# Kernel optimization log

Measured on AMD Instinct MI355X. Metric: run time of the kernel, lower is better.

The kernel has to match this reference:

```python
import jax, jax.numpy as jnp
import numpy as np

FEATURE_DIM = 128  # user_aae.feature_dim == item_aae.feature_dim


def _encode(row, W1, b1, W2, b2):
    # row = [feature | x_rest]; original concatenates x and feature before the encoder MLP
    feat = row[:, :FEATURE_DIM]
    xr = row[:, FEATURE_DIM:]
    h = jax.nn.relu(jnp.concatenate([xr, feat], axis=-1) @ W1 + b1)
    return h @ W2 + b2  # [B, latent]


def setup_inputs() -> dict:
    key = jax.random.key(0)
    ks = jax.random.split(key, 12)
    B, NU, NI = 8192, 50000, 50000
    ROW, H, L = 2128, 512, 256  # feature_dim(128) + x_dim(2000)
    x = jnp.stack([
        jax.random.randint(ks[0], (B,), 0, NU),
        jax.random.randint(ks[1], (B,), 0, NI),
    ], axis=1).astype(jnp.int64)
    s1 = 1.0 / np.sqrt(ROW)
    s2 = 1.0 / np.sqrt(H)
    return {
        "x": x,
        "user_lookup": jax.random.normal(ks[2], (NU, ROW), jnp.float32),
        "item_lookup": jax.random.normal(ks[3], (NI, ROW), jnp.float32),
        "uW1": jax.random.normal(ks[4], (ROW, H), jnp.float32) * s1,
        "ub1": jnp.zeros((H,), jnp.float32),
        "uW2": jax.random.normal(ks[5], (H, L), jnp.float32) * s2,
        "ub2": jnp.zeros((L,), jnp.float32),
        "iW1": jax.random.normal(ks[6], (ROW, H), jnp.float32) * s1,
        "ib1": jnp.zeros((H,), jnp.float32),
        "iW2": jax.random.normal(ks[7], (H, L), jnp.float32) * s2,
        "ib2": jnp.zeros((L,), jnp.float32),
    }


def reference(x, user_lookup, item_lookup, uW1, ub1, uW2, ub2, iW1, ib1, iW2, ib2):
    user_row = user_lookup[x[:, 0]]  # [B, ROW]
    item_row = item_lookup[x[:, 1]]  # [B, ROW]
    u = _encode(user_row, uW1, ub1, uW2, ub2)  # [B, L]
    v = _encode(item_row, iW1, ib1, iW2, ib2)  # [B, L]
    # diag(u @ v.T) == rowwise dot product (identical math, no B x B matrix)
    diag = jnp.sum(u * v, axis=-1)
    return diag[:, None]  # [B, 1]
```

## Files before the change

### kernel.cpp

```cpp
#include <hip/hip_runtime.h>
#include <stdint.h>

typedef __attribute__((ext_vector_type(8))) short bf16x8;
typedef __attribute__((ext_vector_type(4))) float f32x4;

#define MFMA16(a, b, c) __builtin_amdgcn_mfma_f32_16x16x32_bf16((a), (b), (c), 0, 0, 0)

static __device__ __forceinline__ unsigned f2bf(float f) {
  union { float f; unsigned u; } cv;
  cv.f = f;
  return (cv.u + 0x7fffu + ((cv.u >> 16) & 1u)) >> 16;
}

#define BATCH 8192
#define ROWD  2128
#define HID   512
#define LATD  256
#define KC1   272
#define NT1   68
#define HSL_TW (BATCH * HID)

__device__ __forceinline__ void tcast_body(
    const float* __restrict__ in, unsigned short* __restrict__ o,
    int s, int N, int lgN, int Kin, int perm)
{
  const int kc = s >> lgN, n = s & (N - 1);
  unsigned short v[8];
#pragma unroll
  for (int e = 0; e < 8; ++e) {
    const int k = kc * 8 + e;
    float f = 0.0f;
    if (k < Kin) {
      const int src = perm ? (k < 128 ? k + 2000 : k - 128) : k;
      f = in[(size_t)src * N + n];
    }
    v[e] = (unsigned short)f2bf(f);
  }
  *(uint4*)(o + (size_t)s * 8) = *(const uint4*)v;
}

__global__ __launch_bounds__(256) void ASAECF_tcast(
    const float* __restrict__ uW1, const float* __restrict__ iW1,
    const float* __restrict__ uW2, const float* __restrict__ iW2,
    unsigned short* __restrict__ w1s, unsigned short* __restrict__ w2s)
{
  const int tower = blockIdx.z;
  const int s = blockIdx.x * 256 + threadIdx.x;
  if (blockIdx.y == 0) {
    tcast_body(tower ? iW1 : uW1, w1s + (size_t)tower * KC1 * HID * 8,
               s, HID, 9, ROWD, 1);
  } else {
    if (blockIdx.x >= 64) return;
    tcast_body(tower ? iW2 : uW2, w2s + (size_t)tower * 64 * LATD * 8,
               s, LATD, 8, HID, 0);
  }
}

__global__ __launch_bounds__(512) void ASAECF_gemm1(
    const int* __restrict__ x,
    const float* __restrict__ ulook, const float* __restrict__ ilook,
    const unsigned short* __restrict__ w1s,
    const float* __restrict__ ub1, const float* __restrict__ ib1,
    unsigned short* __restrict__ hsl)
{
  const int bid   = blockIdx.x;
  const int xcd   = bid & 7;
  const int idx   = bid >> 3;
  const int tower = xcd >> 2;
  const int nh    = idx & 1;
  const int mb    = (xcd & 3) * 16 + (idx >> 1);

  const float* __restrict__ look = tower ? ilook : ulook;
  const unsigned short* __restrict__ w1 = w1s + (size_t)tower * KC1 * HID * 8;
  const float* __restrict__ b1 = tower ? ib1 : ub1;
  unsigned short* __restrict__ hout = hsl + (size_t)tower * HSL_TW;

  __shared__ unsigned short Ab[2][128 * 40];

  const int tid  = threadIdx.x;
  const int lane = tid & 63, wid = tid >> 6;
  const int fr   = lane & 15, fq = lane >> 4;
  const int row0 = mb * 128;

  const int ar = tid >> 2, ak = (tid & 3) * 8;
  const long long arow = (long long)x[(row0 + ar) * 2 + tower] * ROWD + ak;

  int boff[2];
#pragma unroll
  for (int n = 0; n < 2; ++n)
    boff[n] = (fq * 512 + nh * 256 + wid * 32 + n * 16 + fr) * 8;

  struct A8 { f32x4 a, b; };
  auto loadA = [&](int tt) -> A8 {
    A8 v;
    v.a = f32x4{0.0f, 0.0f, 0.0f, 0.0f};
    v.b = f32x4{0.0f, 0.0f, 0.0f, 0.0f};
    if (tt * 32 + ak + 8 <= ROWD) {
      v.a = *(const f32x4*)(look + arow + tt * 32);
      v.b = *(const f32x4*)(look + arow + tt * 32 + 4);
    }
    return v;
  };
  auto writeA = [&](int buf, A8 v) {
    uint2 p, q;
    p.x = f2bf(v.a[0]) | (f2bf(v.a[1]) << 16);
    p.y = f2bf(v.a[2]) | (f2bf(v.a[3]) << 16);
    q.x = f2bf(v.b[0]) | (f2bf(v.b[1]) << 16);
    q.y = f2bf(v.b[2]) | (f2bf(v.b[3]) << 16);
    *(uint2*)&Ab[buf][ar * 40 + ak] = p;
    *(uint2*)&Ab[buf][ar * 40 + ak + 4] = q;
  };

  f32x4 acc[8][2] = {};
  bf16x8 bgc[2], bgn[2];
  A8 rA0, rA1;

  writeA(0, loadA(0));
  rA0 = loadA(1);
  rA1 = loadA(2);
#pragma unroll
  for (int n = 0; n < 2; ++n) bgc[n] = *(const bf16x8*)(w1 + boff[n]);

#pragma unroll 2
  for (int t = 0; t < NT1; ++t) {
    __syncthreads();
    const int cu = t & 1;

    const unsigned short* bpn = w1 + (size_t)(t + 1) * (4 * 512 * 8);
#pragma unroll
    for (int n = 0; n < 2; ++n) bgn[n] = *(const bf16x8*)(bpn + boff[n]);

    bf16x8 af[8];
#pragma unroll
    for (int m = 0; m < 8; ++m)
      af[m] = *(const bf16x8*)&Ab[cu][(m * 16 + fr) * 40 + fq * 8];
#pragma unroll
    for (int n = 0; n < 2; ++n)
#pragma unroll
      for (int m = 0; m < 8; ++m)
        acc[m][n] = MFMA16(af[m], bgc[n], acc[m][n]);

    if (cu == 0) { writeA(1, rA0); rA0 = loadA(t + 3); }
    else         { writeA(0, rA1); rA1 = loadA(t + 3); }

#pragma unroll
    for (int n = 0; n < 2; ++n) bgc[n] = bgn[n];
  }

#pragma unroll
  for (int n = 0; n < 2; ++n) {
    const int col = nh * 256 + wid * 32 + n * 16 + fr;
    const int kc = col >> 3, e = col & 7;
    const float bb = b1[col];
#pragma unroll
    for (int m = 0; m < 8; ++m)
#pragma unroll
      for (int i = 0; i < 4; ++i) {
        const int rowib = m * 16 + fq * 4 + i;
        const int chunk = mb * 2 + (rowib >> 6);
        const int row = rowib & 63;
        const float v = fmaxf(acc[m][n][i] + bb, 0.0f);
        hout[(((size_t)chunk * 64 + kc) * 64 + row) * 8 + e] = (unsigned short)f2bf(v);
      }
  }
}

__global__ __launch_bounds__(512, 2) void ASAECF_gemm2dot(
    const unsigned short* __restrict__ hsl,
    const unsigned short* __restrict__ w2s,
    const float* __restrict__ ub2, const float* __restrict__ ib2,
    float* __restrict__ out)
{
  const int tid  = threadIdx.x;
  const int lane = tid & 63, wid = tid >> 6;
  const int fr   = lane & 15, fq = lane >> 4;
  const int rb   = blockIdx.x;
  const int row0 = rb * 32;

  const unsigned short* __restrict__ hu = hsl;
  const unsigned short* __restrict__ hv = hsl + (size_t)HSL_TW;
  const size_t abase = ((size_t)(rb >> 1) * 64) * 64 * 8;
  const int lrow0 = (rb & 1) * 32;

  f32x4 au[2][2] = {}, av[2][2] = {};

#pragma unroll
  for (int t = 0; t < 8; ++t) {
#pragma unroll
    for (int s = 0; s < 2; ++s) {
      const int kc = t * 8 + s * 4 + fq;
      bf16x8 a_u[2], a_v[2], b_u[2], b_v[2];
#pragma unroll
      for (int m = 0; m < 2; ++m) {
        const size_t off = abase + ((size_t)kc * 64 + lrow0 + m * 16 + fr) * 8;
        a_u[m] = *(const bf16x8*)(hu + off);
        a_v[m] = *(const bf16x8*)(hv + off);
      }
#pragma unroll
      for (int n = 0; n < 2; ++n) {
        const int col = wid * 32 + n * 16 + fr;
        const size_t offb = ((size_t)kc * 256 + col) * 8;
        b_u[n] = *(const bf16x8*)(w2s + offb);
        b_v[n] = *(const bf16x8*)(w2s + (size_t)64 * 256 * 8 + offb);
      }
#pragma unroll
      for (int m = 0; m < 2; ++m)
#pragma unroll
        for (int n = 0; n < 2; ++n) {
          au[m][n] = MFMA16(a_u[m], b_u[n], au[m][n]);
          av[m][n] = MFMA16(a_v[m], b_v[n], av[m][n]);
        }
    }
  }

  __shared__ float red[8][32];
  float bu[2], bv[2];
#pragma unroll
  for (int n = 0; n < 2; ++n) {
    const int col = wid * 32 + n * 16 + fr;
    bu[n] = ub2[col];
    bv[n] = ib2[col];
  }
#pragma unroll
  for (int m = 0; m < 2; ++m)
#pragma unroll
    for (int i = 0; i < 4; ++i) {
      float p = 0.0f;
#pragma unroll
      for (int n = 0; n < 2; ++n)
        p += (au[m][n][i] + bu[n]) * (av[m][n][i] + bv[n]);
      p += __shfl_xor(p, 1, 64);
      p += __shfl_xor(p, 2, 64);
      p += __shfl_xor(p, 4, 64);
      p += __shfl_xor(p, 8, 64);
      if (fr == 0) red[wid][m * 16 + fq * 4 + i] = p;
    }
  __syncthreads();
  if (tid < 32) {
    float s = 0.0f;
#pragma unroll
    for (int w = 0; w < 8; ++w) s += red[w][tid];
    out[row0 + tid] = s;
  }
}

extern "C" void kernel_launch(void* const* d_in, const int* in_sizes, int n_in,
                              void* d_out, int out_size, void* d_ws, size_t ws_size,
                              hipStream_t stream) {
  (void)in_sizes; (void)n_in; (void)out_size; (void)ws_size;
  const int*   x     = (const int*)d_in[0];
  const float* ulook = (const float*)d_in[1];
  const float* ilook = (const float*)d_in[2];
  const float* uW1   = (const float*)d_in[3];
  const float* ub1   = (const float*)d_in[4];
  const float* uW2   = (const float*)d_in[5];
  const float* ub2   = (const float*)d_in[6];
  const float* iW1   = (const float*)d_in[7];
  const float* ib1   = (const float*)d_in[8];
  const float* iW2   = (const float*)d_in[9];
  const float* ib2   = (const float*)d_in[10];
  float* out = (float*)d_out;

  char* ws = (char*)d_ws;
  unsigned short* w1s = (unsigned short*)(ws);
  unsigned short* w2s = (unsigned short*)(ws + 4456448);
  unsigned short* hsl = (unsigned short*)(ws + 4980736);

  ASAECF_tcast<<<dim3(544, 2, 2), 256, 0, stream>>>(uW1, iW1, uW2, iW2, w1s, w2s);
  ASAECF_gemm1<<<dim3(256), 512, 0, stream>>>(x, ulook, ilook, w1s, ub1, ib1, hsl);
  ASAECF_gemm2dot<<<dim3(256), 512, 0, stream>>>(hsl, w2s, ub2, ib2, out);
}
```

Before: 77.75 us.

## Pre-gather and bf16-cast lookup rows, stage A via direct global-to-LDS loads

Adds a separate kernel that gathers the embedding rows for each batch index and casts them to bf16 into a padded dense workspace buffer. gemm1 then streams A tiles straight into LDS with global_load_lds instead of loading fp32 into registers, converting, and storing. This is meant to halve the A traffic inside the GEMM and remove conversion and register pressure from its main loop. The cost is an extra launch and a round trip of the gathered bf16 matrix through HBM. The unpadded LDS stride may also cause bank conflicts on the fragment reads.

After: 115.9 us. 49.1% more time.

```diff
diff --git a/kernel.cpp b/kernel.cpp
--- a/kernel.cpp
+++ b/kernel.cpp
@@ -5,6 +5,12 @@
 typedef __attribute__((ext_vector_type(4))) float f32x4;
 
 #define MFMA16(a, b, c) __builtin_amdgcn_mfma_f32_16x16x32_bf16((a), (b), (c), 0, 0, 0)
+
+__device__ __forceinline__ void gload_lds16(const void* g, void* l) {
+  __builtin_amdgcn_global_load_lds((const __attribute__((address_space(1))) void*)g,
+                                   (__attribute__((address_space(3))) void*)l,
+                                   16, 0, 0);
+}
 
 static __device__ __forceinline__ unsigned f2bf(float f) {
   union { float f; unsigned u; } cv;
@@ -14,6 +20,7 @@
 
 #define BATCH 8192
 #define ROWD  2128
+#define KP1   2176
 #define HID   512
 #define LATD  256
 #define KC1   272
@@ -56,9 +63,34 @@
   }
 }
 
-__global__ __launch_bounds__(512) void ASAECF_gemm1(
+__global__ __launch_bounds__(256) void ASAECF_agather(
     const int* __restrict__ x,
     const float* __restrict__ ulook, const float* __restrict__ ilook,
+    unsigned short* __restrict__ Ad)
+{
+  const int tower = blockIdx.y;
+  const int row   = blockIdx.x * 4 + (threadIdx.x >> 6);
+  const int lane  = threadIdx.x & 63;
+  const float* __restrict__ look = tower ? ilook : ulook;
+  const long long src = (long long)x[row * 2 + tower] * ROWD;
+  unsigned short* dst = Ad + ((size_t)tower * BATCH + row) * KP1;
+
+#pragma unroll
+  for (int c = 0; c < 9; ++c) {
+    const int k = c * 256 + lane * 4;
+    if (c == 8 && lane >= 32) break;
+    f32x4 v = {0.0f, 0.0f, 0.0f, 0.0f};
+    if (k + 4 <= ROWD)
+      v = __builtin_nontemporal_load((const f32x4*)(look + src + k));
+    uint2 p;
+    p.x = f2bf(v[0]) | (f2bf(v[1]) << 16);
+    p.y = f2bf(v[2]) | (f2bf(v[3]) << 16);
+    *(uint2*)(dst + k) = p;
+  }
+}
+
+__global__ __launch_bounds__(512) void ASAECF_gemm1(
+    const unsigned short* __restrict__ Ad,
     const unsigned short* __restrict__ w1s,
     const float* __restrict__ ub1, const float* __restrict__ ib1,
     unsigned short* __restrict__ hsl)
@@ -70,61 +102,41 @@
   const int nh    = idx & 1;
   const int mb    = (xcd & 3) * 16 + (idx >> 1);
 
-  const float* __restrict__ look = tower ? ilook : ulook;
+  const unsigned short* __restrict__ Adt = Ad + (size_t)tower * BATCH * KP1;
   const unsigned short* __restrict__ w1 = w1s + (size_t)tower * KC1 * HID * 8;
   const float* __restrict__ b1 = tower ? ib1 : ub1;
   unsigned short* __restrict__ hout = hsl + (size_t)tower * HSL_TW;
 
-  __shared__ unsigned short Ab[2][128 * 40];
+  __shared__ unsigned short Ab[2][128 * 32];
 
   const int tid  = threadIdx.x;
   const int lane = tid & 63, wid = tid >> 6;
   const int fr   = lane & 15, fq = lane >> 4;
   const int row0 = mb * 128;
 
-  const int ar = tid >> 2, ak = (tid & 3) * 8;
-  const long long arow = (long long)x[(row0 + ar) * 2 + tower] * ROWD + ak;
+  const unsigned short* asrc =
+      Adt + (size_t)(row0 + wid * 16 + (lane >> 2)) * KP1 + (lane & 3) * 8;
+  auto stageA = [&](int t, int buf) {
+    gload_lds16(asrc + t * 32, (char*)&Ab[buf][0] + wid * 1024 + lane * 16);
+  };
 
   int boff[2];
 #pragma unroll
   for (int n = 0; n < 2; ++n)
     boff[n] = (fq * 512 + nh * 256 + wid * 32 + n * 16 + fr) * 8;
 
-  struct A8 { f32x4 a, b; };
-  auto loadA = [&](int tt) -> A8 {
-    A8 v;
-    v.a = f32x4{0.0f, 0.0f, 0.0f, 0.0f};
-    v.b = f32x4{0.0f, 0.0f, 0.0f, 0.0f};
-    if (tt * 32 + ak + 8 <= ROWD) {
-      v.a = *(const f32x4*)(look + arow + tt * 32);
-      v.b = *(const f32x4*)(look + arow + tt * 32 + 4);
-    }
-    return v;
-  };
-  auto writeA = [&](int buf, A8 v) {
-    uint2 p, q;
-    p.x = f2bf(v.a[0]) | (f2bf(v.a[1]) << 16);
-    p.y = f2bf(v.a[2]) | (f2bf(v.a[3]) << 16);
-    q.x = f2bf(v.b[0]) | (f2bf(v.b[1]) << 16);
-    q.y = f2bf(v.b[2]) | (f2bf(v.b[3]) << 16);
-    *(uint2*)&Ab[buf][ar * 40 + ak] = p;
-    *(uint2*)&Ab[buf][ar * 40 + ak + 4] = q;
-  };
-
   f32x4 acc[8][2] = {};
   bf16x8 bgc[2], bgn[2];
-  A8 rA0, rA1;
-
-  writeA(0, loadA(0));
-  rA0 = loadA(1);
-  rA1 = loadA(2);
+
+  stageA(0, 0);
 #pragma unroll
   for (int n = 0; n < 2; ++n) bgc[n] = *(const bf16x8*)(w1 + boff[n]);
+  __syncthreads();
 
 #pragma unroll 2
   for (int t = 0; t < NT1; ++t) {
-    __syncthreads();
     const int cu = t & 1;
+    if (t + 1 < NT1) stageA(t + 1, cu ^ 1);
 
     const unsigned short* bpn = w1 + (size_t)(t + 1) * (4 * 512 * 8);
 #pragma unroll
@@ -133,18 +145,17 @@
     bf16x8 af[8];
 #pragma unroll
     for (int m = 0; m < 8; ++m)
-      af[m] = *(const bf16x8*)&Ab[cu][(m * 16 + fr) * 40 + fq * 8];
+      af[m] = *(const bf16x8*)&Ab[cu][(m * 16 + fr) * 32 + fq * 8];
 #pragma unroll
     for (int n = 0; n < 2; ++n)
 #pragma unroll
       for (int m = 0; m < 8; ++m)
         acc[m][n] = MFMA16(af[m], bgc[n], acc[m][n]);
 
-    if (cu == 0) { writeA(1, rA0); rA0 = loadA(t + 3); }
-    else         { writeA(0, rA1); rA1 = loadA(t + 3); }
-
 #pragma unroll
     for (int n = 0; n < 2; ++n) bgc[n] = bgn[n];
+
+    __syncthreads();
   }
 
 #pragma unroll
@@ -265,8 +276,10 @@
   unsigned short* w1s = (unsigned short*)(ws);
   unsigned short* w2s = (unsigned short*)(ws + 4456448);
   unsigned short* hsl = (unsigned short*)(ws + 4980736);
+  unsigned short* Ad  = (unsigned short*)(ws + 21757952);
 
   ASAECF_tcast<<<dim3(544, 2, 2), 256, 0, stream>>>(uW1, iW1, uW2, iW2, w1s, w2s);
-  ASAECF_gemm1<<<dim3(256), 512, 0, stream>>>(x, ulook, ilook, w1s, ub1, ib1, hsl);
+  ASAECF_agather<<<dim3(2048, 2), 256, 0, stream>>>(x, ulook, ilook, Ad);
+  ASAECF_gemm1<<<dim3(256), 512, 0, stream>>>(Ad, w1s, ub1, ib1, hsl);
   ASAECF_gemm2dot<<<dim3(256), 512, 0, stream>>>(hsl, w2s, ub2, ib2, out);
 }
```

## Widen gemm1 K-step to 128 with larger LDS double buffers

Applied to the files above, without the earlier changes.

The gather-GEMM main loop now advances 128 K elements per iteration instead of 32, giving 17 iterations instead of 68. Each thread loads 32 contiguous floats per gathered row and prefetches four B slabs into registers. This cuts the number of block-wide barriers and issues longer contiguous gather loads, so more memory is in flight per round trip. In exchange it needs 80KB of dynamic LDS and many more registers per thread, which may lower occupancy or cause spills.

New measurement: 110.6 us. +42.3%, slower.

```diff
diff --git a/kernel.cpp b/kernel.cpp
--- a/kernel.cpp
+++ b/kernel.cpp
@@ -17,7 +17,10 @@
 #define HID   512
 #define LATD  256
 #define KC1   272
-#define NT1   68
+#define NTB   17
+#define SLAB  16384
+#define SUBT  5120
+#define ABUF  20480
 #define HSL_TW (BATCH * HID)
 
 __device__ __forceinline__ void tcast_body(
@@ -63,6 +66,8 @@
     const float* __restrict__ ub1, const float* __restrict__ ib1,
     unsigned short* __restrict__ hsl)
 {
+  extern __shared__ unsigned short Asl[];
+
   const int bid   = blockIdx.x;
   const int xcd   = bid & 7;
   const int idx   = bid >> 3;
@@ -75,76 +80,89 @@
   const float* __restrict__ b1 = tower ? ib1 : ub1;
   unsigned short* __restrict__ hout = hsl + (size_t)tower * HSL_TW;
 
-  __shared__ unsigned short Ab[2][128 * 40];
-
   const int tid  = threadIdx.x;
   const int lane = tid & 63, wid = tid >> 6;
   const int fr   = lane & 15, fq = lane >> 4;
   const int row0 = mb * 128;
 
-  const int ar = tid >> 2, ak = (tid & 3) * 8;
-  const long long arow = (long long)x[(row0 + ar) * 2 + tower] * ROWD + ak;
+  const int ar = tid >> 2, ks0 = tid & 3;
+  const long long arow = (long long)x[(row0 + ar) * 2 + tower] * ROWD + ks0 * 32;
+  unsigned short* awr = &Asl[0] ;
 
   int boff[2];
 #pragma unroll
   for (int n = 0; n < 2; ++n)
     boff[n] = (fq * 512 + nh * 256 + wid * 32 + n * 16 + fr) * 8;
 
-  struct A8 { f32x4 a, b; };
-  auto loadA = [&](int tt) -> A8 {
-    A8 v;
-    v.a = f32x4{0.0f, 0.0f, 0.0f, 0.0f};
-    v.b = f32x4{0.0f, 0.0f, 0.0f, 0.0f};
-    if (tt * 32 + ak + 8 <= ROWD) {
-      v.a = *(const f32x4*)(look + arow + tt * 32);
-      v.b = *(const f32x4*)(look + arow + tt * 32 + 4);
-    }
-    return v;
+  f32x4 rA[8];
+  auto loadA = [&](int t) {
+    const int kb = t * 128 + ks0 * 32;
+#pragma unroll
+    for (int j = 0; j < 8; ++j) {
+      rA[j] = f32x4{0.0f, 0.0f, 0.0f, 0.0f};
+      if (kb + j * 4 + 4 <= ROWD)
+        rA[j] = *(const f32x4*)(look + arow + t * 128 + j * 4);
+    }
   };
-  auto writeA = [&](int buf, A8 v) {
-    uint2 p, q;
-    p.x = f2bf(v.a[0]) | (f2bf(v.a[1]) << 16);
-    p.y = f2bf(v.a[2]) | (f2bf(v.a[3]) << 16);
-    q.x = f2bf(v.b[0]) | (f2bf(v.b[1]) << 16);
-    q.y = f2bf(v.b[2]) | (f2bf(v.b[3]) << 16);
-    *(uint2*)&Ab[buf][ar * 40 + ak] = p;
-    *(uint2*)&Ab[buf][ar * 40 + ak + 4] = q;
+  auto writeA = [&](int buf) {
+    unsigned short v[32];
+#pragma unroll
+    for (int j = 0; j < 8; ++j)
+#pragma unroll
+      for (int e = 0; e < 4; ++e)
+        v[j * 4 + e] = (unsigned short)f2bf(rA[j][e]);
+    unsigned short* d = &Asl[buf * ABUF + ks0 * SUBT + ar * 40];
+#pragma unroll
+    for (int c = 0; c < 4; ++c)
+      *(bf16x8*)(d + c * 8) = *(const bf16x8*)(v + c * 8);
   };
 
   f32x4 acc[8][2] = {};
-  bf16x8 bgc[2], bgn[2];
-  A8 rA0, rA1;
-
-  writeA(0, loadA(0));
-  rA0 = loadA(1);
-  rA1 = loadA(2);
-#pragma unroll
-  for (int n = 0; n < 2; ++n) bgc[n] = *(const bf16x8*)(w1 + boff[n]);
-
-#pragma unroll 2
-  for (int t = 0; t < NT1; ++t) {
+  bf16x8 Bc[4][2], Bn[4][2];
+
+  loadA(0);
+  writeA(0);
+#pragma unroll
+  for (int s = 0; s < 4; ++s)
+#pragma unroll
+    for (int n = 0; n < 2; ++n)
+      Bc[s][n] = *(const bf16x8*)(w1 + (size_t)s * SLAB + boff[n]);
+  __syncthreads();
+
+  for (int t = 0; t < NTB; ++t) {
+    const int cu = t & 1;
+    const bool pre = (t + 1 < NTB);
+    if (pre) {
+#pragma unroll
+      for (int s = 0; s < 4; ++s)
+#pragma unroll
+        for (int n = 0; n < 2; ++n)
+          Bn[s][n] = *(const bf16x8*)(w1 + (size_t)((t + 1) * 4 + s) * SLAB + boff[n]);
+      loadA(t + 1);
+    }
+
+#pragma unroll
+    for (int s = 0; s < 4; ++s) {
+      bf16x8 af[8];
+#pragma unroll
+      for (int m = 0; m < 8; ++m)
+        af[m] = *(const bf16x8*)&Asl[cu * ABUF + s * SUBT + (m * 16 + fr) * 40 + fq * 8];
+#pragma unroll
+      for (int n = 0; n < 2; ++n)
+#pragma unroll
+        for (int m = 0; m < 8; ++m)
+          acc[m][n] = MFMA16(af[m], Bc[s][n], acc[m][n]);
+    }
+
+    if (pre) {
+      writeA(cu ^ 1);
+#pragma unroll
+      for (int s = 0; s < 4; ++s)
+#pragma unroll
+        for (int n = 0; n < 2; ++n)
+          Bc[s][n] = Bn[s][n];
+    }
     __syncthreads();
-    const int cu = t & 1;
-
-    const unsigned short* bpn = w1 + (size_t)(t + 1) * (4 * 512 * 8);
-#pragma unroll
-    for (int n = 0; n < 2; ++n) bgn[n] = *(const bf16x8*)(bpn + boff[n]);
-
-    bf16x8 af[8];
-#pragma unroll
-    for (int m = 0; m < 8; ++m)
-      af[m] = *(const bf16x8*)&Ab[cu][(m * 16 + fr) * 40 + fq * 8];
-#pragma unroll
-    for (int n = 0; n < 2; ++n)
-#pragma unroll
-      for (int m = 0; m < 8; ++m)
-        acc[m][n] = MFMA16(af[m], bgc[n], acc[m][n]);
-
-    if (cu == 0) { writeA(1, rA0); rA0 = loadA(t + 3); }
-    else         { writeA(0, rA1); rA1 = loadA(t + 3); }
-
-#pragma unroll
-    for (int n = 0; n < 2; ++n) bgc[n] = bgn[n];
   }
 
 #pragma unroll
@@ -267,6 +285,6 @@
   unsigned short* hsl = (unsigned short*)(ws + 4980736);
 
   ASAECF_tcast<<<dim3(544, 2, 2), 256, 0, stream>>>(uW1, iW1, uW2, iW2, w1s, w2s);
-  ASAECF_gemm1<<<dim3(256), 512, 0, stream>>>(x, ulook, ilook, w1s, ub1, ib1, hsl);
+  ASAECF_gemm1<<<dim3(256), 512, 81920, stream>>>(x, ulook, ilook, w1s, ub1, ib1, hsl);
   ASAECF_gemm2dot<<<dim3(256), 512, 0, stream>>>(hsl, w2s, ub2, ib2, out);
 }
```

## Split gemm1 K dimension in two halves and combine partials in gemm2

Applied to the files above, without the earlier changes.

The first GEMM is split along K into two halves, doubling the grid from 256 to 512 blocks so more CUs are occupied. Each half writes bf16 partial sums to a separate buffer, with the bias added only by the first half. The second kernel loads both partials, sums them, and applies ReLU before its MFMA. This trades extra hidden-activation traffic and an extra bf16 rounding of partial sums for more parallelism in the dominant GEMM.

After: 189.8 us. +144.2%, slower.

```diff
diff --git a/kernel.cpp b/kernel.cpp
--- a/kernel.cpp
+++ b/kernel.cpp
@@ -17,7 +17,7 @@
 #define HID   512
 #define LATD  256
 #define KC1   272
-#define NT1   68
+#define NTH   34
 #define HSL_TW (BATCH * HID)
 
 __device__ __forceinline__ void tcast_body(
@@ -56,24 +56,26 @@
   }
 }
 
-__global__ __launch_bounds__(512) void ASAECF_gemm1(
+__global__ __launch_bounds__(512, 4) void ASAECF_gemm1(
     const int* __restrict__ x,
     const float* __restrict__ ulook, const float* __restrict__ ilook,
     const unsigned short* __restrict__ w1s,
     const float* __restrict__ ub1, const float* __restrict__ ib1,
-    unsigned short* __restrict__ hsl)
+    unsigned short* __restrict__ hp0, unsigned short* __restrict__ hp1)
 {
   const int bid   = blockIdx.x;
   const int xcd   = bid & 7;
   const int idx   = bid >> 3;
   const int tower = xcd >> 2;
-  const int nh    = idx & 1;
-  const int mb    = (xcd & 3) * 16 + (idx >> 1);
+  const int kh    = idx & 1;
+  const int nh    = (idx >> 1) & 1;
+  const int mb    = (xcd & 3) * 16 + (idx >> 2);
 
   const float* __restrict__ look = tower ? ilook : ulook;
   const unsigned short* __restrict__ w1 = w1s + (size_t)tower * KC1 * HID * 8;
   const float* __restrict__ b1 = tower ? ib1 : ub1;
-  unsigned short* __restrict__ hout = hsl + (size_t)tower * HSL_TW;
+  unsigned short* __restrict__ hout =
+      (kh ? hp1 : hp0) + (size_t)tower * HSL_TW;
 
   __shared__ unsigned short Ab[2][128 * 40];
 
@@ -115,14 +117,16 @@
   bf16x8 bgc[2], bgn[2];
   A8 rA0, rA1;
 
-  writeA(0, loadA(0));
-  rA0 = loadA(1);
-  rA1 = loadA(2);
-#pragma unroll
-  for (int n = 0; n < 2; ++n) bgc[n] = *(const bf16x8*)(w1 + boff[n]);
+  const int t0 = kh * NTH;
+  writeA(0, loadA(t0));
+  rA0 = loadA(t0 + 1);
+  rA1 = loadA(t0 + 2);
+#pragma unroll
+  for (int n = 0; n < 2; ++n)
+    bgc[n] = *(const bf16x8*)(w1 + (size_t)t0 * (4 * 512 * 8) + boff[n]);
 
 #pragma unroll 2
-  for (int t = 0; t < NT1; ++t) {
+  for (int t = t0; t < t0 + NTH; ++t) {
     __syncthreads();
     const int cu = t & 1;
 
@@ -140,8 +144,8 @@
       for (int m = 0; m < 8; ++m)
         acc[m][n] = MFMA16(af[m], bgc[n], acc[m][n]);
 
-    if (cu == 0) { writeA(1, rA0); rA0 = loadA(t + 3); }
-    else         { writeA(0, rA1); rA1 = loadA(t + 3); }
+    if (cu == (t0 & 1)) { writeA(1 ^ (t0 & 1), rA0); rA0 = loadA(t + 3); }
+    else                { writeA(t0 & 1, rA1);       rA1 = loadA(t + 3); }
 
 #pragma unroll
     for (int n = 0; n < 2; ++n) bgc[n] = bgn[n];
@@ -151,7 +155,7 @@
   for (int n = 0; n < 2; ++n) {
     const int col = nh * 256 + wid * 32 + n * 16 + fr;
     const int kc = col >> 3, e = col & 7;
-    const float bb = b1[col];
+    const float bb = kh ? 0.0f : b1[col];
 #pragma unroll
     for (int m = 0; m < 8; ++m)
 #pragma unroll
@@ -159,14 +163,15 @@
         const int rowib = m * 16 + fq * 4 + i;
         const int chunk = mb * 2 + (rowib >> 6);
         const int row = rowib & 63;
-        const float v = fmaxf(acc[m][n][i] + bb, 0.0f);
-        hout[(((size_t)chunk * 64 + kc) * 64 + row) * 8 + e] = (unsigned short)f2bf(v);
+        hout[(((size_t)chunk * 64 + kc) * 64 + row) * 8 + e] =
+            (unsigned short)f2bf(acc[m][n][i] + bb);
       }
   }
 }
 
 __global__ __launch_bounds__(512, 2) void ASAECF_gemm2dot(
-    const unsigned short* __restrict__ hsl,
+    const unsigned short* __restrict__ hp0,
+    const unsigned short* __restrict__ hp1,
     const unsigned short* __restrict__ w2s,
     const float* __restrict__ ub2, const float* __restrict__ ib2,
     float* __restrict__ out)
@@ -177,10 +182,25 @@
   const int rb   = blockIdx.x;
   const int row0 = rb * 32;
 
-  const unsigned short* __restrict__ hu = hsl;
-  const unsigned short* __restrict__ hv = hsl + (size_t)HSL_TW;
   const size_t abase = ((size_t)(rb >> 1) * 64) * 64 * 8;
   const int lrow0 = (rb & 1) * 32;
+
+  auto combine = [&](bf16x8 p0, bf16x8 p1) -> bf16x8 {
+    union { bf16x8 v; unsigned u[4]; } a, b, r;
+    a.v = p0; b.v = p1;
+#pragma unroll
+    for (int j = 0; j < 4; ++j) {
+      union { float f; unsigned u; } x0, x1, y0, y1;
+      x0.u = a.u[j] << 16;       x1.u = a.u[j] & 0xffff0000u;
+      y0.u = b.u[j] << 16;       y1.u = b.u[j] & 0xffff0000u;
+      float lo = fmaxf(x0.f + y0.f, 0.0f);
+      float hi = fmaxf(x1.f + y1.f, 0.0f);
+      union { float f; unsigned u; } lu, hu2;
+      lu.f = lo; hu2.f = hi;
+      r.u[j] = (lu.u >> 16) | (hu2.u & 0xffff0000u);
+    }
+    return r.v;
+  };
 
   f32x4 au[2][2] = {}, av[2][2] = {};
 
@@ -193,8 +213,10 @@
 #pragma unroll
       for (int m = 0; m < 2; ++m) {
         const size_t off = abase + ((size_t)kc * 64 + lrow0 + m * 16 + fr) * 8;
-        a_u[m] = *(const bf16x8*)(hu + off);
-        a_v[m] = *(const bf16x8*)(hv + off);
+        a_u[m] = combine(*(const bf16x8*)(hp0 + off),
+                         *(const bf16x8*)(hp1 + off));
+        a_v[m] = combine(*(const bf16x8*)(hp0 + (size_t)HSL_TW + off),
+                         *(const bf16x8*)(hp1 + (size_t)HSL_TW + off));
       }
 #pragma unroll
       for (int n = 0; n < 2; ++n) {
@@ -264,9 +286,10 @@
   char* ws = (char*)d_ws;
   unsigned short* w1s = (unsigned short*)(ws);
   unsigned short* w2s = (unsigned short*)(ws + 4456448);
-  unsigned short* hsl = (unsigned short*)(ws + 4980736);
+  unsigned short* hp0 = (unsigned short*)(ws + 4980736);
+  unsigned short* hp1 = (unsigned short*)(ws + 21757952);
 
   ASAECF_tcast<<<dim3(544, 2, 2), 256, 0, stream>>>(uW1, iW1, uW2, iW2, w1s, w2s);
-  ASAECF_gemm1<<<dim3(256), 512, 0, stream>>>(x, ulook, ilook, w1s, ub1, ib1, hsl);
-  ASAECF_gemm2dot<<<dim3(256), 512, 0, stream>>>(hsl, w2s, ub2, ib2, out);
-}
+  ASAECF_gemm1<<<dim3(512), 512, 0, stream>>>(x, ulook, ilook, w1s, ub1, ib1, hp0, hp1);
+  ASAECF_gemm2dot<<<dim3(256), 512, 0, stream>>>(hp0, hp1, w2s, ub2, ib2, out);
+}
```
